# Kernel optimization log

Hardware: AMD Instinct MI355X
Metric: run time of the kernel (lower is better)

## Reference

```python
import jax, jax.numpy as jnp
import numpy as np

D_MODEL, D_STATE, D_CONV, EXPAND = 1024, 16, 4, 2
D_INNER = D_MODEL * EXPAND


def setup_inputs() -> dict:
    key = jax.random.key(0)
    ks = jax.random.split(key, 12)
    s = lambda fan_in: 1.0 / np.sqrt(fan_in)
    return {
        "x": jax.random.normal(ks[0], (2, 2048, D_MODEL), dtype=jnp.float32),
        "W_in": jax.random.normal(ks[1], (D_MODEL, 2 * D_INNER), dtype=jnp.float32) * s(D_MODEL),
        "b_in": jnp.zeros((2 * D_INNER,), jnp.float32),
        "W_conv": jax.random.normal(ks[2], (D_INNER, 1, D_CONV), dtype=jnp.float32) * s(D_CONV),
        "b_conv": jnp.zeros((D_INNER,), jnp.float32),
        "A_log": jax.random.normal(ks[3], (D_INNER, D_STATE), dtype=jnp.float32) * -0.5 - 1.0,
        "D": jnp.ones((D_INNER,), jnp.float32),
        "W_B": jax.random.normal(ks[4], (D_INNER, D_STATE), dtype=jnp.float32) * s(D_INNER),
        "b_B": jnp.zeros((D_STATE,), jnp.float32),
        "W_C": jax.random.normal(ks[5], (D_INNER, D_STATE), dtype=jnp.float32) * s(D_INNER),
        "b_C": jnp.zeros((D_STATE,), jnp.float32),
        "W_out": jax.random.normal(ks[6], (D_INNER, D_MODEL), dtype=jnp.float32) * s(D_INNER),
        "b_out": jnp.zeros((D_MODEL,), jnp.float32),
    }


def reference(x, W_in, b_in, W_conv, b_conv, A_log, D, W_B, b_B, W_C, b_C, W_out, b_out):
    B, L, _ = x.shape
    xz = x @ W_in + b_in                       # (B, L, 2*D_INNER)
    xi, z = jnp.split(xz, 2, axis=-1)
    # depthwise causal conv1d (left pad d_conv-1, truncate to L)
    xc = jnp.swapaxes(xi, 1, 2)                # (B, D_INNER, L)
    xc = jax.lax.conv_general_dilated(
        xc, W_conv, window_strides=(1,), padding=[(D_CONV - 1, 0)],
        dimension_numbers=("NCH", "OIH", "NCH"), feature_group_count=D_INNER)
    xc = xc + b_conv[None, :, None]
    xi = jnp.swapaxes(xc, 1, 2)                # (B, L, D_INNER)
    xi = jax.nn.silu(xi)

    A = -jnp.exp(jnp.clip(A_log, -10.0, 2.0))  # (D_INNER, D_STATE)
    Bm = xi @ W_B + b_B                        # (B, L, D_STATE)
    Cm = xi @ W_C + b_C                        # (B, L, D_STATE)

    def step(h, inp):
        x_t, B_t, C_t = inp                    # (B,D_INNER), (B,D_STATE), (B,D_STATE)
        h = h * A[None] + x_t[:, :, None] * B_t[:, None, :]
        h = jnp.clip(h, -100.0, 100.0)
        y = jnp.einsum("bds,bs->bd", h, C_t) + D * x_t
        y = jnp.clip(y, -100.0, 100.0)
        return h, y

    h0 = jnp.zeros((B, D_INNER, D_STATE), x.dtype)
    xs = (jnp.swapaxes(xi, 0, 1), jnp.swapaxes(Bm, 0, 1), jnp.swapaxes(Cm, 0, 1))
    _, ys = jax.lax.scan(step, h0, xs)         # ys: (L, B, D_INNER)
    y = jnp.swapaxes(ys, 0, 1)                 # (B, L, D_INNER)
    y = y * jax.nn.sigmoid(z)
    return y @ W_out + b_out
```

## Files before the change

### kernel.cpp

```cpp
#include <hip/hip_runtime.h>
#include <hip/hip_bf16.h>
#include <math.h>

#define B_SZ   2
#define L_SZ   2048
#define DM     1024
#define DI     2048
#define DS     16
#define M_SZ   (B_SZ * L_SZ)
#define N_XZ   (2 * DI)
#define LDF    20

typedef short bf16x8 __attribute__((ext_vector_type(8)));
typedef float f32x4  __attribute__((ext_vector_type(4)));

__device__ __forceinline__ unsigned short rne16(float f) {
  unsigned int u = __builtin_bit_cast(unsigned int, f);
  u += 0x7FFFu + ((u >> 16) & 1u);
  return (unsigned short)(u >> 16);
}
__device__ __forceinline__ float frombf(unsigned short h) {
  unsigned int u = ((unsigned int)h) << 16;
  return __builtin_bit_cast(float, u);
}

__global__ __launch_bounds__(256) void convert_x(
    const float* __restrict__ x, unsigned short* __restrict__ xh,
    unsigned short* __restrict__ xl) {
  int i = (blockIdx.x * 256 + threadIdx.x) * 4;
  float4 v = *(const float4*)(x + i);
  unsigned short h0 = rne16(v.x), h1 = rne16(v.y), h2 = rne16(v.z), h3 = rne16(v.w);
  *(ushort4*)(xh + i) = make_ushort4(h0, h1, h2, h3);
  *(ushort4*)(xl + i) = make_ushort4(rne16(v.x - frombf(h0)), rne16(v.y - frombf(h1)),
                                     rne16(v.z - frombf(h2)), rne16(v.w - frombf(h3)));
}

__global__ __launch_bounds__(256) void transpose_w(
    const float* __restrict__ in, int R, int C,
    unsigned short* __restrict__ oh, unsigned short* __restrict__ ol) {
  __shared__ float T[64][65];
  const int tid = threadIdx.x;
  const int c0 = blockIdx.x * 64, r0 = blockIdx.y * 64;
  const int cc = tid & 63, rq = tid >> 6;
  #pragma unroll
  for (int i = 0; i < 16; ++i) {
    int r = rq * 16 + i;
    T[r][cc] = in[(size_t)(r0 + r) * C + c0 + cc];
  }
  __syncthreads();
  #pragma unroll
  for (int i = 0; i < 16; ++i) {
    int c = rq * 16 + i;
    float v = T[cc][c];
    size_t o = (size_t)(c0 + c) * R + r0 + cc;
    unsigned short h = rne16(v);
    oh[o] = h;
    if (ol) ol[o] = rne16(v - frombf(h));
  }
}

template<int BN, bool X3, bool OUTBF16>
__global__ __launch_bounds__(256, X3 ? 3 : 4) void gemm_t(
    const unsigned short* __restrict__ Ah, const unsigned short* __restrict__ Al, int lda,
    const unsigned short* __restrict__ Bh, const unsigned short* __restrict__ Bl, int ldb,
    const float* __restrict__ bias, float* __restrict__ Cf,
    unsigned short* __restrict__ Cz, int ldc, int K) {
  constexpr int WN  = BN / 2;
  constexpr int FJ  = BN / 32;
  constexpr int BCH = BN / 64;
  __shared__ unsigned int AhS[128 * LDF];
  __shared__ unsigned int BhS[BN * LDF];
  __shared__ unsigned int AlS[X3 ? 128 * LDF : 4];
  __shared__ unsigned int BlS[X3 ? BN * LDF : 4];
  const int tid  = threadIdx.x;
  const int lane = tid & 63, wave = tid >> 6;
  const int wr = wave >> 1, wc = wave & 1;
  const int lm = lane & 15, lq = lane >> 4;
  const int row0 = blockIdx.y * 128, col0 = blockIdx.x * BN;

  f32x4 acc[4][FJ];
  #pragma unroll
  for (int i = 0; i < 4; ++i)
    #pragma unroll
    for (int j = 0; j < FJ; ++j) acc[i][j] = (f32x4){0.f, 0.f, 0.f, 0.f};

  for (int k0 = 0; k0 < K; k0 += 32) {
    __syncthreads();
    #pragma unroll
    for (int i = 0; i < 2; ++i) {
      int idx = tid + i * 256, r = idx >> 2, q = idx & 3;
      size_t go = (size_t)(row0 + r) * lda + k0 + q * 8;
      *(uint4*)&AhS[r * LDF + q * 4] = *(const uint4*)(Ah + go);
      if constexpr (X3)
        *(uint4*)&AlS[r * LDF + q * 4] = *(const uint4*)(Al + go);
    }
    #pragma unroll
    for (int i = 0; i < BCH; ++i) {
      int idx = tid + i * 256, r = idx >> 2, q = idx & 3;
      size_t go = (size_t)(col0 + r) * ldb + k0 + q * 8;
      *(uint4*)&BhS[r * LDF + q * 4] = *(const uint4*)(Bh + go);
      if constexpr (X3)
        *(uint4*)&BlS[r * LDF + q * 4] = *(const uint4*)(Bl + go);
    }
    __syncthreads();
    bf16x8 bh[FJ], bl[FJ];
    #pragma unroll
    for (int j = 0; j < FJ; ++j) {
      bh[j] = *(const bf16x8*)&BhS[(wc * WN + j * 16 + lm) * LDF + lq * 4];
      if constexpr (X3)
        bl[j] = *(const bf16x8*)&BlS[(wc * WN + j * 16 + lm) * LDF + lq * 4];
    }
    #pragma unroll
    for (int i = 0; i < 4; ++i) {
      bf16x8 ah = *(const bf16x8*)&AhS[(wr * 64 + i * 16 + lm) * LDF + lq * 4];
      bf16x8 al;
      if constexpr (X3)
        al = *(const bf16x8*)&AlS[(wr * 64 + i * 16 + lm) * LDF + lq * 4];
      #pragma unroll
      for (int j = 0; j < FJ; ++j) {
        acc[i][j] = __builtin_amdgcn_mfma_f32_16x16x32_bf16(ah, bh[j], acc[i][j], 0, 0, 0);
        if constexpr (X3) {
          acc[i][j] = __builtin_amdgcn_mfma_f32_16x16x32_bf16(ah, bl[j], acc[i][j], 0, 0, 0);
          acc[i][j] = __builtin_amdgcn_mfma_f32_16x16x32_bf16(al, bh[j], acc[i][j], 0, 0, 0);
        }
      }
    }
  }
  #pragma unroll
  for (int i = 0; i < 4; ++i) {
    #pragma unroll
    for (int j = 0; j < FJ; ++j) {
      int c = col0 + wc * WN + j * 16 + lm;
      float bs = bias[c];
      #pragma unroll
      for (int k = 0; k < 4; ++k) {
        int r = row0 + wr * 64 + i * 16 + lq * 4 + k;
        float v = acc[i][j][k] + bs;
        if constexpr (OUTBF16) Cz[(size_t)r * ldc + c] = rne16(v);
        else                   Cf[(size_t)r * ldc + c] = v;
      }
    }
  }
}

__global__ __launch_bounds__(256) void conv_silu_kernel(
    const float* __restrict__ xi, const float* __restrict__ Wc,
    const float* __restrict__ bc, float* __restrict__ xc) {
  int idx = blockIdx.x * blockDim.x + threadIdx.x;
  if (idx >= M_SZ * DI) return;
  int d  = idx & (DI - 1);
  int bl = idx >> 11;
  int l  = bl & (L_SZ - 1);
  float4 w = ((const float4*)Wc)[d];
  const float* base = xi + (size_t)bl * DI + d;
  float s = bc[d] + base[0] * w.w;
  if (l >= 1) s = fmaf(base[-DI],     w.z, s);
  if (l >= 2) s = fmaf(base[-2 * DI], w.y, s);
  if (l >= 3) s = fmaf(base[-3 * DI], w.x, s);
  float sig = 1.f / (1.f + expf(-s));
  xc[idx] = s * sig;
}

__global__ __launch_bounds__(256) void gemm_bc_kernel(
    const float* __restrict__ xc,
    const float* __restrict__ WB, const float* __restrict__ bB,
    const float* __restrict__ WC, const float* __restrict__ bC,
    float* __restrict__ Bm, float* __restrict__ Cm) {
  int t = blockIdx.x * blockDim.x + threadIdx.x;
  int row = t >> 5;
  int cc  = t & 31;
  int s   = cc & 15;
  const float* W = (cc < 16) ? WB : WC;
  const float4* xr4 = (const float4*)(xc + (size_t)row * DI);
  float acc = 0.f;
  #pragma unroll 4
  for (int k4 = 0; k4 < DI / 4; ++k4) {
    float4 xv = xr4[k4];
    int k = k4 * 4;
    acc = fmaf(xv.x, W[(k    ) * DS + s], acc);
    acc = fmaf(xv.y, W[(k + 1) * DS + s], acc);
    acc = fmaf(xv.z, W[(k + 2) * DS + s], acc);
    acc = fmaf(xv.w, W[(k + 3) * DS + s], acc);
  }
  if (cc < 16) Bm[row * DS + s] = acc + bB[s];
  else         Cm[row * DS + s] = acc + bC[s];
}

#define WCH    4
#define SCH    16
#define CHUNK  64
#define XSTR   66
#define PSTR   68
#define BCF    (CHUNK * 32)
#define PSF    (16 * PSTR)
#define WLDSF  (WCH * XSTR + BCF + PSF + CHUNK * 4)

__global__ __launch_bounds__(256) void scan_kernel(
    const float* __restrict__ xc, const unsigned short* __restrict__ zb,
    const float* __restrict__ Bm, const float* __restrict__ Cm,
    const float* __restrict__ A_log, const float* __restrict__ Dv,
    unsigned short* __restrict__ yg) {
  const int b    = blockIdx.y;
  const int tid  = threadIdx.x;
  const int wave = tid >> 6;
  const int lane = tid & 63;
  const int dd   = lane >> 4;
  const int s    = lane & 15;
  const int lr   = lane >> 2;
  const int ddr  = lane & 3;
  const int dw0  = blockIdx.x * SCH + wave * WCH;

  __shared__ float SM[4 * WLDSF];
  float* Xs2 = SM + wave * WLDSF;
  float* BCs = Xs2 + WCH * XSTR;
  float* Ps  = BCs + BCF;
  float* yS  = Ps + PSF;

  float Alog = A_log[(dw0 + dd) * DS + s];
  Alog = fminf(fmaxf(Alog, -10.f), 2.f);
  const float A  = -expf(Alog);
  const float Dr = Dv[dw0 + ddr];
  float h = 0.f;

  const size_t rbase = (size_t)b * L_SZ;

  float4 pX, pB[4], pC[4];
  uint2 pZ;
  {
    size_t row = rbase + lane;
    pX = *(const float4*)(xc + row * DI + dw0);
    pZ = *(const uint2*)(zb + row * DI + dw0);
    #pragma unroll
    for (int i = 0; i < 4; ++i) {
      int idx = lane + i * 64;
      size_t rr = rbase + (idx >> 2);
      pB[i] = *(const float4*)(Bm + rr * DS + (idx & 3) * 4);
      pC[i] = *(const float4*)(Cm + rr * DS + (idx & 3) * 4);
    }
  }

  for (int l0 = 0; l0 < L_SZ; l0 += CHUNK) {
    __builtin_amdgcn_s_barrier();
    Xs2[0 * XSTR + lane] = pX.x;
    Xs2[1 * XSTR + lane] = pX.y;
    Xs2[2 * XSTR + lane] = pX.z;
    Xs2[3 * XSTR + lane] = pX.w;
    #pragma unroll
    for (int i = 0; i < 4; ++i) {
      int idx = lane + i * 64;
      float* bb = BCs + idx * 8;
      *(float2*)(bb + 0) = make_float2(pB[i].x, pC[i].x);
      *(float2*)(bb + 2) = make_float2(pB[i].y, pC[i].y);
      *(float2*)(bb + 4) = make_float2(pB[i].z, pC[i].z);
      *(float2*)(bb + 6) = make_float2(pB[i].w, pC[i].w);
    }
    const uint2 zc = pZ;
    if (l0 + CHUNK < L_SZ) {
      size_t row = rbase + l0 + CHUNK + lane;
      pX = *(const float4*)(xc + row * DI + dw0);
      pZ = *(const uint2*)(zb + row * DI + dw0);
      #pragma unroll
      for (int i = 0; i < 4; ++i) {
        int idx = lane + i * 64;
        size_t rr = rbase + l0 + CHUNK + (idx >> 2);
        pB[i] = *(const float4*)(Bm + rr * DS + (idx & 3) * 4);
        pC[i] = *(const float4*)(Cm + rr * DS + (idx & 3) * 4);
      }
    }
    #pragma unroll
    for (int q = 0; q < 4; ++q) {
      #pragma unroll
      for (int u = 0; u < 16; u += 2) {
        const int l = q * 16 + u;
        float2 x2  = *(const float2*)&Xs2[dd * XSTR + l];
        float2 bc0 = *(const float2*)&BCs[l * 32 + s * 2];
        float2 bc1 = *(const float2*)&BCs[(l + 1) * 32 + s * 2];
        h = fmaf(h, A, x2.x * bc0.x);
        h = fminf(fmaxf(h, -100.f), 100.f);
        float p0 = h * bc0.y;
        h = fmaf(h, A, x2.y * bc1.x);
        h = fminf(fmaxf(h, -100.f), 100.f);
        float p1 = h * bc1.y;
        Ps[u * PSTR + lane]       = p0;
        Ps[(u + 1) * PSTR + lane] = p1;
      }
      asm volatile("" ::: "memory");
      const float* pp = Ps + lr * PSTR + ddr * 16;
      float4 a0 = *(const float4*)(pp + 0);
      float4 a1 = *(const float4*)(pp + 4);
      float4 a2 = *(const float4*)(pp + 8);
      float4 a3 = *(const float4*)(pp + 12);
      float t0 = (a0.x + a0.y) + (a0.z + a0.w);
      float t1 = (a1.x + a1.y) + (a1.z + a1.w);
      float t2 = (a2.x + a2.y) + (a2.z + a2.w);
      float t3 = (a3.x + a3.y) + (a3.z + a3.w);
      float sum = (t0 + t1) + (t2 + t3);
      const int lg = q * 16 + lr;
      float xv = Xs2[ddr * XSTR + lg];
      float y  = fmaf(Dr, xv, sum);
      y = fminf(fmaxf(y, -100.f), 100.f);
      yS[lg * 4 + ddr] = y;
      asm volatile("" ::: "memory");
    }
    float4 yv = *(const float4*)&yS[lane * 4];
    float zf0 = frombf((unsigned short)(zc.x & 0xFFFF));
    float zf1 = frombf((unsigned short)(zc.x >> 16));
    float zf2 = frombf((unsigned short)(zc.y & 0xFFFF));
    float zf3 = frombf((unsigned short)(zc.y >> 16));
    ushort4 o;
    o.x = rne16(yv.x * (1.f / (1.f + expf(-zf0))));
    o.y = rne16(yv.y * (1.f / (1.f + expf(-zf1))));
    o.z = rne16(yv.z * (1.f / (1.f + expf(-zf2))));
    o.w = rne16(yv.w * (1.f / (1.f + expf(-zf3))));
    *(ushort4*)(yg + (rbase + l0 + lane) * DI + dw0) = o;
  }
}

extern "C" void kernel_launch(void* const* d_in, const int* in_sizes, int n_in,
                              void* d_out, int out_size, void* d_ws, size_t ws_size,
                              hipStream_t stream) {
  const float* x      = (const float*)d_in[0];
  const float* W_in   = (const float*)d_in[1];
  const float* b_in   = (const float*)d_in[2];
  const float* W_conv = (const float*)d_in[3];
  const float* b_conv = (const float*)d_in[4];
  const float* A_log  = (const float*)d_in[5];
  const float* Dv     = (const float*)d_in[6];
  const float* W_B    = (const float*)d_in[7];
  const float* b_B    = (const float*)d_in[8];
  const float* W_C    = (const float*)d_in[9];
  const float* b_C    = (const float*)d_in[10];
  const float* W_out  = (const float*)d_in[11];
  const float* b_out  = (const float*)d_in[12];
  float* out = (float*)d_out;

  char* w = (char*)d_ws;
  float*          xi   = (float*)(w + 0);
  unsigned short* yg   = (unsigned short*)(w + 0);
  unsigned short* zb   = (unsigned short*)(w + 33554432);
  float*          xc   = (float*)(w + 50331648);
  unsigned short* xh   = (unsigned short*)(w + 50331648);
  unsigned short* xl   = (unsigned short*)(w + 58720256);
  unsigned short* WhT  = (unsigned short*)(w + 67108864);
  unsigned short* WlT  = (unsigned short*)(w + 75497472);
  float*          Bm   = (float*)(w + 83886080);
  float*          Cm   = (float*)(w + 84148224);
  unsigned short* WoT  = (unsigned short*)(w + 84410368);

  convert_x<<<M_SZ * DM / 1024, 256, 0, stream>>>(x, xh, xl);
  transpose_w<<<dim3(N_XZ / 64, DM / 64), 256, 0, stream>>>(W_in, DM, N_XZ, WhT, WlT);
  transpose_w<<<dim3(DM / 64, DI / 64), 256, 0, stream>>>(W_out, DI, DM, WoT, nullptr);

  gemm_t<128, true, false><<<dim3(DI / 128, M_SZ / 128), 256, 0, stream>>>(
      xh, xl, DM, WhT, WlT, DM, b_in, xi, nullptr, DI, DM);

  gemm_t<128, false, true><<<dim3(DI / 128, M_SZ / 128), 256, 0, stream>>>(
      xh, nullptr, DM, WhT + (size_t)DI * DM, nullptr, DM,
      b_in + DI, nullptr, zb, DI, DM);

  conv_silu_kernel<<<M_SZ * DI / 256, 256, 0, stream>>>(xi, W_conv, b_conv, xc);

  gemm_bc_kernel<<<M_SZ * 32 / 256, 256, 0, stream>>>(xc, W_B, b_B, W_C, b_C, Bm, Cm);

  scan_kernel<<<dim3(DI / SCH, B_SZ), 256, 0, stream>>>(xc, zb, Bm, Cm, A_log, Dv, yg);

  gemm_t<64, false, false><<<dim3(DM / 64, M_SZ / 128), 256, 0, stream>>>(
      yg, nullptr, DI, WoT, nullptr, DI, b_out, out, nullptr, DM, DI);
}
```

Baseline: 435.2 us.

## Split selective scan into boundary-state pass and segment-parallel output pass

Replaces the single sequential scan kernel with two kernels. The first runs a lighter recurrence over the first three quarters of the sequence and stores the state at each 512-step boundary. The second then processes four segments in parallel, each starting from its stored state, giving four times as many blocks. It also interleaves B and C into one buffer, broadcasts x with ds_swizzle instead of LDS staging, folds the D*x skip term into the per-state reduction, and loads z inside the loop. The cost is a second sequential pass over most of the sequence plus extra reads of xc and B/C.

```diff
diff --git a/kernel.cpp b/kernel.cpp
--- a/kernel.cpp
+++ b/kernel.cpp
@@ -10,6 +10,9 @@
 #define M_SZ   (B_SZ * L_SZ)
 #define N_XZ   (2 * DI)
 #define LDF    20
+#define SEGS   4
+#define SEGLEN 512
+#define PSTR   68
 
 typedef short bf16x8 __attribute__((ext_vector_type(8)));
 typedef float f32x4  __attribute__((ext_vector_type(4)));
@@ -165,7 +168,7 @@
     const float* __restrict__ xc,
     const float* __restrict__ WB, const float* __restrict__ bB,
     const float* __restrict__ WC, const float* __restrict__ bC,
-    float* __restrict__ Bm, float* __restrict__ Cm) {
+    float* __restrict__ BCm) {
   int t = blockIdx.x * blockDim.x + threadIdx.x;
   int row = t >> 5;
   int cc  = t & 31;
@@ -182,109 +185,128 @@
     acc = fmaf(xv.z, W[(k + 2) * DS + s], acc);
     acc = fmaf(xv.w, W[(k + 3) * DS + s], acc);
   }
-  if (cc < 16) Bm[row * DS + s] = acc + bB[s];
-  else         Cm[row * DS + s] = acc + bC[s];
-}
-
-#define WCH    4
-#define SCH    16
-#define CHUNK  64
-#define XSTR   66
-#define PSTR   68
-#define BCF    (CHUNK * 32)
-#define PSF    (16 * PSTR)
-#define WLDSF  (WCH * XSTR + BCF + PSF + CHUNK * 4)
-
-__global__ __launch_bounds__(256) void scan_kernel(
-    const float* __restrict__ xc, const unsigned short* __restrict__ zb,
-    const float* __restrict__ Bm, const float* __restrict__ Cm,
+  if (cc < 16) BCm[row * 32 + s * 2]     = acc + bB[s];
+  else         BCm[row * 32 + s * 2 + 1] = acc + bC[s];
+}
+
+
+#define SWZ_BCAST16(k, xr) \
+  __builtin_bit_cast(float, __builtin_amdgcn_ds_swizzle( \
+      __builtin_bit_cast(int, (xr)), ((k) << 5) | 0x10))
+
+#define P1STEP(k, xr, bb) { \
+  float xk = SWZ_BCAST16(k, xr); \
+  h = fmaf(h, A, xk * (bb)[k]); \
+  h = fminf(fmaxf(h, -100.f), 100.f); }
+
+#define P1WIN(xr, bb) \
+  P1STEP(0, xr, bb)  P1STEP(1, xr, bb)  P1STEP(2, xr, bb)  P1STEP(3, xr, bb) \
+  P1STEP(4, xr, bb)  P1STEP(5, xr, bb)  P1STEP(6, xr, bb)  P1STEP(7, xr, bb) \
+  P1STEP(8, xr, bb)  P1STEP(9, xr, bb)  P1STEP(10, xr, bb) P1STEP(11, xr, bb) \
+  P1STEP(12, xr, bb) P1STEP(13, xr, bb) P1STEP(14, xr, bb) P1STEP(15, xr, bb)
+
+__global__ __launch_bounds__(256, 4) void scan_pass1(
+    const float* __restrict__ xc, const float* __restrict__ BCm,
+    const float* __restrict__ A_log, float* __restrict__ hseg) {
+  const int b    = blockIdx.y;
+  const int wave = threadIdx.x >> 6;
+  const int lane = threadIdx.x & 63;
+  const int dd   = lane >> 4, s = lane & 15;
+  const int d    = blockIdx.x * 16 + wave * 4 + dd;
+
+  float Alog = A_log[d * DS + s];
+  Alog = fminf(fmaxf(Alog, -10.f), 2.f);
+  const float A = -expf(Alog);
+  float h = 0.f;
+
+  const float* px = xc  + (size_t)b * L_SZ * DI + d;
+  const float* pb = BCm + (size_t)b * L_SZ * 32 + s * 2;
+
+  float xrA, xrB, bA[16], bB16[16];
+  {
+    xrA = px[s * DI];
+    #pragma unroll
+    for (int j = 0; j < 16; ++j) bA[j] = pb[j * 32];
+  }
+  for (int g = 0; g < 96; g += 2) {
+    {
+      const int t0 = (g + 1) * 16;
+      xrB = px[(t0 + s) * DI];
+      #pragma unroll
+      for (int j = 0; j < 16; ++j) bB16[j] = pb[(t0 + j) * 32];
+    }
+    P1WIN(xrA, bA)
+    if (g + 2 < 96) {
+      const int t0 = (g + 2) * 16;
+      xrA = px[(t0 + s) * DI];
+      #pragma unroll
+      for (int j = 0; j < 16; ++j) bA[j] = pb[(t0 + j) * 32];
+    }
+    P1WIN(xrB, bB16)
+    if (((g + 1) & 31) == 31)
+      hseg[(((size_t)b * 3 + ((g + 1) >> 5)) * DI + d) * DS + s] = h;
+  }
+}
+
+#define P2STEP(k, xr, bc) { \
+  float xk = SWZ_BCAST16(k, xr); \
+  h = fmaf(h, A, xk * (bc)[k].x); \
+  h = fminf(fmaxf(h, -100.f), 100.f); \
+  Ps[(k) * PSTR + lane] = fmaf(dsel, xk, h * (bc)[k].y); }
+
+#define P2WIN(xr, bc) \
+  P2STEP(0, xr, bc)  P2STEP(1, xr, bc)  P2STEP(2, xr, bc)  P2STEP(3, xr, bc) \
+  P2STEP(4, xr, bc)  P2STEP(5, xr, bc)  P2STEP(6, xr, bc)  P2STEP(7, xr, bc) \
+  P2STEP(8, xr, bc)  P2STEP(9, xr, bc)  P2STEP(10, xr, bc) P2STEP(11, xr, bc) \
+  P2STEP(12, xr, bc) P2STEP(13, xr, bc) P2STEP(14, xr, bc) P2STEP(15, xr, bc)
+
+__global__ __launch_bounds__(256, 4) void scan_pass2(
+    const float* __restrict__ xc, const float* __restrict__ BCm,
+    const unsigned short* __restrict__ zb,
     const float* __restrict__ A_log, const float* __restrict__ Dv,
-    unsigned short* __restrict__ yg) {
-  const int b    = blockIdx.y;
-  const int tid  = threadIdx.x;
-  const int wave = tid >> 6;
-  const int lane = tid & 63;
-  const int dd   = lane >> 4;
-  const int s    = lane & 15;
-  const int lr   = lane >> 2;
-  const int ddr  = lane & 3;
-  const int dw0  = blockIdx.x * SCH + wave * WCH;
-
-  __shared__ float SM[4 * WLDSF];
-  float* Xs2 = SM + wave * WLDSF;
-  float* BCs = Xs2 + WCH * XSTR;
-  float* Ps  = BCs + BCF;
-  float* yS  = Ps + PSF;
+    const float* __restrict__ hseg, unsigned short* __restrict__ yg) {
+  const int b    = blockIdx.y >> 2;
+  const int seg  = blockIdx.y & 3;
+  const int wave = threadIdx.x >> 6;
+  const int lane = threadIdx.x & 63;
+  const int dd   = lane >> 4, s = lane & 15;
+  const int lr   = lane >> 2, ddr = lane & 3;
+  const int dw0  = blockIdx.x * 16 + wave * 4;
+
+  __shared__ float SM[4 * (16 * PSTR + 256)];
+  float* Ps = SM + wave * (16 * PSTR + 256);
+  float* yS = Ps + 16 * PSTR;
 
   float Alog = A_log[(dw0 + dd) * DS + s];
   Alog = fminf(fmaxf(Alog, -10.f), 2.f);
-  const float A  = -expf(Alog);
-  const float Dr = Dv[dw0 + ddr];
+  const float A    = -expf(Alog);
+  const float dsel = (s == 0) ? Dv[dw0 + dd] : 0.f;
+
   float h = 0.f;
-
-  const size_t rbase = (size_t)b * L_SZ;
-
-  float4 pX, pB[4], pC[4];
-  uint2 pZ;
+  if (seg > 0)
+    h = hseg[(((size_t)b * 3 + (seg - 1)) * DI + dw0 + dd) * DS + s];
+
+  const int rbase = b * L_SZ + seg * SEGLEN;
+  const float* px  = xc  + (size_t)rbase * DI + dw0 + dd;
+  const float* pbc = BCm + (size_t)rbase * 32 + s * 2;
+
+  float  xrA, xrB;
+  float2 bcA[16], bcB[16];
   {
-    size_t row = rbase + lane;
-    pX = *(const float4*)(xc + row * DI + dw0);
-    pZ = *(const uint2*)(zb + row * DI + dw0);
-    #pragma unroll
-    for (int i = 0; i < 4; ++i) {
-      int idx = lane + i * 64;
-      size_t rr = rbase + (idx >> 2);
-      pB[i] = *(const float4*)(Bm + rr * DS + (idx & 3) * 4);
-      pC[i] = *(const float4*)(Cm + rr * DS + (idx & 3) * 4);
-    }
-  }
-
-  for (int l0 = 0; l0 < L_SZ; l0 += CHUNK) {
-    __builtin_amdgcn_s_barrier();
-    Xs2[0 * XSTR + lane] = pX.x;
-    Xs2[1 * XSTR + lane] = pX.y;
-    Xs2[2 * XSTR + lane] = pX.z;
-    Xs2[3 * XSTR + lane] = pX.w;
-    #pragma unroll
-    for (int i = 0; i < 4; ++i) {
-      int idx = lane + i * 64;
-      float* bb = BCs + idx * 8;
-      *(float2*)(bb + 0) = make_float2(pB[i].x, pC[i].x);
-      *(float2*)(bb + 2) = make_float2(pB[i].y, pC[i].y);
-      *(float2*)(bb + 4) = make_float2(pB[i].z, pC[i].z);
-      *(float2*)(bb + 6) = make_float2(pB[i].w, pC[i].w);
-    }
-    const uint2 zc = pZ;
-    if (l0 + CHUNK < L_SZ) {
-      size_t row = rbase + l0 + CHUNK + lane;
-      pX = *(const float4*)(xc + row * DI + dw0);
-      pZ = *(const uint2*)(zb + row * DI + dw0);
-      #pragma unroll
-      for (int i = 0; i < 4; ++i) {
-        int idx = lane + i * 64;
-        size_t rr = rbase + l0 + CHUNK + (idx >> 2);
-        pB[i] = *(const float4*)(Bm + rr * DS + (idx & 3) * 4);
-        pC[i] = *(const float4*)(Cm + rr * DS + (idx & 3) * 4);
-      }
-    }
-    #pragma unroll
-    for (int q = 0; q < 4; ++q) {
-      #pragma unroll
-      for (int u = 0; u < 16; u += 2) {
-        const int l = q * 16 + u;
-        float2 x2  = *(const float2*)&Xs2[dd * XSTR + l];
-        float2 bc0 = *(const float2*)&BCs[l * 32 + s * 2];
-        float2 bc1 = *(const float2*)&BCs[(l + 1) * 32 + s * 2];
-        h = fmaf(h, A, x2.x * bc0.x);
-        h = fminf(fmaxf(h, -100.f), 100.f);
-        float p0 = h * bc0.y;
-        h = fmaf(h, A, x2.y * bc1.x);
-        h = fminf(fmaxf(h, -100.f), 100.f);
-        float p1 = h * bc1.y;
-        Ps[u * PSTR + lane]       = p0;
-        Ps[(u + 1) * PSTR + lane] = p1;
-      }
-      asm volatile("" ::: "memory");
+    xrA = px[s * DI];
+    #pragma unroll
+    for (int j = 0; j < 16; ++j) bcA[j] = *(const float2*)(pbc + j * 32);
+  }
+  for (int w = 0; w < 32; w += 2) {
+    {
+      const int t0 = (w + 1) * 16;
+      xrB = px[(t0 + s) * DI];
+      #pragma unroll
+      for (int j = 0; j < 16; ++j) bcB[j] = *(const float2*)(pbc + (t0 + j) * 32);
+    }
+    P2WIN(xrA, bcA)
+    asm volatile("" ::: "memory");
+    {
       const float* pp = Ps + lr * PSTR + ddr * 16;
       float4 a0 = *(const float4*)(pp + 0);
       float4 a1 = *(const float4*)(pp + 4);
@@ -294,25 +316,51 @@
       float t1 = (a1.x + a1.y) + (a1.z + a1.w);
       float t2 = (a2.x + a2.y) + (a2.z + a2.w);
       float t3 = (a3.x + a3.y) + (a3.z + a3.w);
-      float sum = (t0 + t1) + (t2 + t3);
-      const int lg = q * 16 + lr;
-      float xv = Xs2[ddr * XSTR + lg];
-      float y  = fmaf(Dr, xv, sum);
+      float y = (t0 + t1) + (t2 + t3);
       y = fminf(fmaxf(y, -100.f), 100.f);
-      yS[lg * 4 + ddr] = y;
+      yS[((w & 3) * 16 + lr) * 4 + ddr] = y;
+    }
+    asm volatile("" ::: "memory");
+    if (w + 2 < 32) {
+      const int t0 = (w + 2) * 16;
+      xrA = px[(t0 + s) * DI];
+      #pragma unroll
+      for (int j = 0; j < 16; ++j) bcA[j] = *(const float2*)(pbc + (t0 + j) * 32);
+    }
+    P2WIN(xrB, bcB)
+    asm volatile("" ::: "memory");
+    {
+      const float* pp = Ps + lr * PSTR + ddr * 16;
+      float4 a0 = *(const float4*)(pp + 0);
+      float4 a1 = *(const float4*)(pp + 4);
+      float4 a2 = *(const float4*)(pp + 8);
+      float4 a3 = *(const float4*)(pp + 12);
+      float t0 = (a0.x + a0.y) + (a0.z + a0.w);
+      float t1 = (a1.x + a1.y) + (a1.z + a1.w);
+      float t2 = (a2.x + a2.y) + (a2.z + a2.w);
+      float t3 = (a3.x + a3.y) + (a3.z + a3.w);
+      float y = (t0 + t1) + (t2 + t3);
+      y = fminf(fmaxf(y, -100.f), 100.f);
+      yS[(((w + 1) & 3) * 16 + lr) * 4 + ddr] = y;
+    }
+    asm volatile("" ::: "memory");
+    if (((w + 1) & 3) == 3) {
+      const int l0 = ((w + 1) - 3) * 16;
+      float4 yv = *(const float4*)&yS[lane * 4];
+      const int row = rbase + l0 + lane;
+      uint2 zB = *(const uint2*)(zb + (size_t)row * DI + dw0);
+      float zf0 = frombf((unsigned short)(zB.x & 0xFFFF));
+      float zf1 = frombf((unsigned short)(zB.x >> 16));
+      float zf2 = frombf((unsigned short)(zB.y & 0xFFFF));
+      float zf3 = frombf((unsigned short)(zB.y >> 16));
+      ushort4 o;
+      o.x = rne16(yv.x * (1.f / (1.f + expf(-zf0))));
+      o.y = rne16(yv.y * (1.f / (1.f + expf(-zf1))));
+      o.z = rne16(yv.z * (1.f / (1.f + expf(-zf2))));
+      o.w = rne16(yv.w * (1.f / (1.f + expf(-zf3))));
+      *(ushort4*)(yg + (size_t)row * DI + dw0) = o;
       asm volatile("" ::: "memory");
     }
-    float4 yv = *(const float4*)&yS[lane * 4];
-    float zf0 = frombf((unsigned short)(zc.x & 0xFFFF));
-    float zf1 = frombf((unsigned short)(zc.x >> 16));
-    float zf2 = frombf((unsigned short)(zc.y & 0xFFFF));
-    float zf3 = frombf((unsigned short)(zc.y >> 16));
-    ushort4 o;
-    o.x = rne16(yv.x * (1.f / (1.f + expf(-zf0))));
-    o.y = rne16(yv.y * (1.f / (1.f + expf(-zf1))));
-    o.z = rne16(yv.z * (1.f / (1.f + expf(-zf2))));
-    o.w = rne16(yv.w * (1.f / (1.f + expf(-zf3))));
-    *(ushort4*)(yg + (rbase + l0 + lane) * DI + dw0) = o;
   }
 }
 
@@ -337,14 +385,14 @@
   char* w = (char*)d_ws;
   float*          xi   = (float*)(w + 0);
   unsigned short* yg   = (unsigned short*)(w + 0);
+  float*          hseg = (float*)(w + 16777216);
+  float*          BCm  = (float*)(w + 17825792);
   unsigned short* zb   = (unsigned short*)(w + 33554432);
   float*          xc   = (float*)(w + 50331648);
   unsigned short* xh   = (unsigned short*)(w + 50331648);
   unsigned short* xl   = (unsigned short*)(w + 58720256);
   unsigned short* WhT  = (unsigned short*)(w + 67108864);
   unsigned short* WlT  = (unsigned short*)(w + 75497472);
-  float*          Bm   = (float*)(w + 83886080);
-  float*          Cm   = (float*)(w + 84148224);
   unsigned short* WoT  = (unsigned short*)(w + 84410368);
 
   convert_x<<<M_SZ * DM / 1024, 256, 0, stream>>>(x, xh, xl);
@@ -360,9 +408,12 @@
 
   conv_silu_kernel<<<M_SZ * DI / 256, 256, 0, stream>>>(xi, W_conv, b_conv, xc);
 
-  gemm_bc_kernel<<<M_SZ * 32 / 256, 256, 0, stream>>>(xc, W_B, b_B, W_C, b_C, Bm, Cm);
-
-  scan_kernel<<<dim3(DI / SCH, B_SZ), 256, 0, stream>>>(xc, zb, Bm, Cm, A_log, Dv, yg);
+  gemm_bc_kernel<<<M_SZ * 32 / 256, 256, 0, stream>>>(xc, W_B, b_B, W_C, b_C, BCm);
+
+  scan_pass1<<<dim3(DI / 16, B_SZ), 256, 0, stream>>>(xc, BCm, A_log, hseg);
+
+  scan_pass2<<<dim3(DI / 16, B_SZ * SEGS), 256, 0, stream>>>(
+      xc, BCm, zb, A_log, Dv, hseg, yg);
 
   gemm_t<64, false, false><<<dim3(DM / 64, M_SZ / 128), 256, 0, stream>>>(
       yg, nullptr, DI, WoT, nullptr, DI, b_out, out, nullptr, DM, DI);
```

Result: slower. 480.7 us (+10.5%).
